# Kernel optimization log

Measured on AMD Instinct MI355X. Metric: run time of the kernel, lower is better.

The kernel has to match this reference:

```python
import jax, jax.numpy as jnp
import numpy as np


def gcn_conv(x, row, col, W, b, n_nodes):
    """PyG GCNConv: x' = D^-1/2 (A+I) D^-1/2 (x W) + b, with self-loops in row/col."""
    xw = x @ W  # [N, out]
    deg = jax.ops.segment_sum(jnp.ones_like(col, dtype=xw.dtype), col, num_segments=n_nodes)
    d_inv_sqrt = jnp.where(deg > 0, jax.lax.rsqrt(deg), 0.0)
    norm = d_inv_sqrt[row] * d_inv_sqrt[col]  # [E+N]
    msgs = norm[:, None] * xw[row]            # gather + scale
    out = jax.ops.segment_sum(msgs, col, num_segments=n_nodes)  # scatter-add to dst
    return out + b


def setup_inputs() -> dict:
    key = jax.random.key(0)
    ks = jax.random.split(key, 8)
    N, E = 100000, 1600000
    d_in, d_h, d_out = 128, 128, 64
    x = jax.random.normal(ks[0], (N, d_in), dtype=jnp.float32)
    edge_index = jax.random.randint(ks[1], (2, E), 0, N, dtype=jnp.int32)
    s = 1.0 / np.sqrt(d_in)
    W1 = jax.random.uniform(ks[2], (d_in, d_h), jnp.float32, -s, s)
    b1 = jnp.zeros((d_h,), jnp.float32)
    sh = 1.0 / np.sqrt(d_h)
    W2 = jax.random.uniform(ks[3], (d_h, d_h), jnp.float32, -sh, sh)
    b2 = jnp.zeros((d_h,), jnp.float32)
    W3 = jax.random.uniform(ks[4], (d_h, d_out), jnp.float32, -sh, sh)
    b3 = jnp.zeros((d_out,), jnp.float32)
    return {"x": x, "edge_index": edge_index, "W1": W1, "b1": b1,
            "W2": W2, "b2": b2, "W3": W3, "b3": b3}


def reference(x, edge_index, W1, b1, W2, b2, W3, b3):
    n_nodes = x.shape[0]
    loops = jnp.arange(n_nodes, dtype=edge_index.dtype)
    row = jnp.concatenate([edge_index[0], loops])  # src (with self-loops)
    col = jnp.concatenate([edge_index[1], loops])  # dst (with self-loops)
    # dropout p=0.0 / eval mode -> identity, omitted
    h = jax.nn.relu(gcn_conv(x, row, col, W1, b1, n_nodes))
    h = jax.nn.relu(gcn_conv(h, row, col, W2, b2, n_nodes))
    out = gcn_conv(h, row, col, W3, b3, n_nodes)
    return out
```

## Files before the change

### kernel.cpp

```cpp
#include <hip/hip_runtime.h>
#include <hip/hip_fp16.h>

typedef _Float16 half8 __attribute__((ext_vector_type(8)));
typedef float floatx4 __attribute__((ext_vector_type(4)));

#define NCH 128
#define TILE 2048
#define CSLOT 48
#define MAXNB 1024
#define MAXCH 1024
#define OVFCAP 65536

__global__ __launch_bounds__(256) void wconv_k(const float* __restrict__ W1,
                                               const float* __restrict__ W2,
                                               const float* __restrict__ W3,
                                               __half* __restrict__ Wt1,
                                               __half* __restrict__ Wt2,
                                               __half* __restrict__ Wt3,
                                               int* __restrict__ ovfcnt) {
    int idx = blockIdx.x * 256 + threadIdx.x;
    if (idx < 16384) {
        int k = idx >> 7, nn = idx & 127;
        Wt1[nn * 128 + k] = __float2half(W1[idx]);
    } else if (idx < 32768) {
        int j = idx - 16384;
        int k = j >> 7, nn = j & 127;
        Wt2[nn * 128 + k] = __float2half(W2[j]);
    } else if (idx < 40960) {
        int j = idx - 32768;
        int k = j >> 6, nn = j & 63;
        Wt3[nn * 128 + k] = __float2half(W3[j]);
    } else if (idx == 40960) {
        *ovfcnt = 0;
    }
}

__global__ __launch_bounds__(256) void part_k(const int* __restrict__ row,
                                              const int* __restrict__ col, int E,
                                              int chunk, int NB,
                                              int* __restrict__ stg_d,
                                              int* __restrict__ stg_s,
                                              int* __restrict__ cnts,
                                              unsigned long long* __restrict__ ovf,
                                              int* __restrict__ ovfcnt) {
    __shared__ int bd[NCH][CSLOT];
    __shared__ int bs[NCH][CSLOT];
    __shared__ int lcnt[NCH];
    __shared__ int lpref[NCH + 1];
    int tid = threadIdx.x;
    int b = blockIdx.x;
    for (int i = tid; i < NCH; i += 256) lcnt[i] = 0;
    __syncthreads();

    int i0 = b * TILE + tid * 8;
    int sv[8], dv[8];
    int nv = 0;
    if (i0 + 7 < E && (E & 3) == 0) {
        int4 r0 = *(const int4*)(row + i0);
        int4 r1 = *(const int4*)(row + i0 + 4);
        int4 c0 = *(const int4*)(col + i0);
        int4 c1 = *(const int4*)(col + i0 + 4);
        sv[0] = r0.x; sv[1] = r0.y; sv[2] = r0.z; sv[3] = r0.w;
        sv[4] = r1.x; sv[5] = r1.y; sv[6] = r1.z; sv[7] = r1.w;
        dv[0] = c0.x; dv[1] = c0.y; dv[2] = c0.z; dv[3] = c0.w;
        dv[4] = c1.x; dv[5] = c1.y; dv[6] = c1.z; dv[7] = c1.w;
        nv = 8;
    } else {
#pragma unroll
        for (int j = 0; j < 8; j++) {
            if (i0 + j < E) { sv[nv] = row[i0 + j]; dv[nv] = col[i0 + j]; nv++; }
        }
    }
#pragma unroll 8
    for (int j = 0; j < nv; j++) {
        int d = dv[j], s = sv[j];
        int c = d / chunk;
        int r = atomicAdd(&lcnt[c], 1);
        if (r < CSLOT) {
            bd[c][r] = d;
            bs[c][r] = s;
        } else {
            int o = atomicAdd(ovfcnt, 1);
            if (o < OVFCAP)
                ovf[o] = ((unsigned long long)(unsigned)d << 32) | (unsigned)s;
        }
    }
    __syncthreads();
    if (tid == 0) {
        int a = 0;
#pragma unroll
        for (int c = 0; c < NCH; c++) {
            lpref[c] = a;
            a += min(lcnt[c], CSLOT);
        }
        lpref[NCH] = a;
    }
    __syncthreads();
    for (int c = tid; c < NCH; c += 256) cnts[(size_t)c * NB + b] = min(lcnt[c], CSLOT);
    int total = lpref[NCH];
    for (int f = tid; f < total; f += 256) {
        int lo = 0, hi = NCH;
        while (hi - lo > 1) {
            int mid = (lo + hi) >> 1;
            if (lpref[mid] <= f) lo = mid; else hi = mid;
        }
        int slot = f - lpref[lo];
        size_t cell = ((size_t)lo * NB + b) * CSLOT;
        stg_d[cell + slot] = bd[lo][slot];
        stg_s[cell + slot] = bs[lo][slot];
    }
}

__global__ __launch_bounds__(256) void degcnt_k(const int* __restrict__ stg_d,
                                                const int* __restrict__ cnts, int NB,
                                                int N, int chunk,
                                                const unsigned long long* __restrict__ ovf,
                                                const int* __restrict__ ovfcnt,
                                                int* __restrict__ deg,
                                                float* __restrict__ dinv) {
    __shared__ int hist[MAXCH];
    __shared__ int lc[MAXNB];
    int c = blockIdx.x, tid = threadIdx.x;
    int dlo = c * chunk;
    int dhi = min(N, dlo + chunk);
    int csz = dhi - dlo;
    if (csz <= 0) return;
    for (int i = tid; i < csz; i += 256) hist[i] = 1;
    for (int i = tid; i < NB; i += 256) lc[i] = cnts[(size_t)c * NB + i];
    __syncthreads();
    for (int b0 = tid >> 4; b0 < NB; b0 += 16) {
        int cnt = lc[b0];
        size_t base = ((size_t)c * NB + b0) * CSLOT;
        for (int slot = tid & 15; slot < cnt; slot += 16) {
            int d = stg_d[base + slot];
            atomicAdd(&hist[d - dlo], 1);
        }
    }
    __syncthreads();
    int oc = min(*ovfcnt, OVFCAP);
    for (int i = tid; i < oc; i += 256) {
        int d = (int)(ovf[i] >> 32);
        if (d >= dlo && d < dhi) atomicAdd(&hist[d - dlo], 1);
    }
    __syncthreads();
    for (int i = tid; i < csz; i += 256) {
        int dg = hist[i];
        deg[dlo + i] = dg;
        dinv[dlo + i] = rsqrtf((float)dg);
    }
}

__global__ __launch_bounds__(256) void scan_p1(const int* __restrict__ deg, int n,
                                               int* __restrict__ bsum) {
    __shared__ int lds[256];
    int t = threadIdx.x;
    int base = blockIdx.x * 1024 + t * 4;
    int s = 0;
#pragma unroll
    for (int i = 0; i < 4; i++) {
        int idx = base + i;
        if (idx < n) s += deg[idx];
    }
    lds[t] = s;
    __syncthreads();
    for (int o = 128; o > 0; o >>= 1) {
        if (t < o) lds[t] += lds[t + o];
        __syncthreads();
    }
    if (t == 0) bsum[blockIdx.x] = lds[0];
}

__global__ __launch_bounds__(256) void scan_p2(int* __restrict__ bsum, int nb) {
    __shared__ int lds[256];
    int t = threadIdx.x;
    int v = (t < nb) ? bsum[t] : 0;
    lds[t] = v;
    __syncthreads();
    for (int o = 1; o < 256; o <<= 1) {
        int tmp = 0;
        if (t >= o) tmp = lds[t - o];
        __syncthreads();
        lds[t] += tmp;
        __syncthreads();
    }
    if (t < nb) bsum[t] = lds[t] - v;
}

__global__ __launch_bounds__(256) void scan_p3(const int* __restrict__ deg, int n,
                                               const int* __restrict__ bsum,
                                               int* __restrict__ cptr) {
    __shared__ int lds[256];
    int t = threadIdx.x;
    int base = blockIdx.x * 1024 + t * 4;
    int v[4];
    int s = 0;
#pragma unroll
    for (int i = 0; i < 4; i++) {
        int idx = base + i;
        v[i] = (idx < n) ? deg[idx] : 0;
        s += v[i];
    }
    lds[t] = s;
    __syncthreads();
    for (int o = 1; o < 256; o <<= 1) {
        int tmp = 0;
        if (t >= o) tmp = lds[t - o];
        __syncthreads();
        lds[t] += tmp;
        __syncthreads();
    }
    int off = bsum[blockIdx.x] + (lds[t] - s);
#pragma unroll
    for (int i = 0; i < 4; i++) {
        int idx = base + i;
        if (idx < n) {
            cptr[idx] = off;
            off += v[i];
            if (idx == n - 1) cptr[n] = off;
        }
    }
}

__global__ __launch_bounds__(256) void fill3_k(const int* __restrict__ stg_d,
                                               const int* __restrict__ stg_s,
                                               const int* __restrict__ cnts, int NB,
                                               const int* __restrict__ cptr,
                                               int N, int chunk,
                                               const unsigned long long* __restrict__ ovf,
                                               const int* __restrict__ ovfcnt,
                                               int* __restrict__ meta) {
    __shared__ int cur[MAXCH];
    __shared__ int lc[MAXNB];
    int c = blockIdx.x, tid = threadIdx.x;
    int dlo = c * chunk;
    int dhi = min(N, dlo + chunk);
    int csz = dhi - dlo;
    if (csz <= 0) return;
    for (int i = tid; i < csz; i += 256) cur[i] = cptr[dlo + i];
    for (int i = tid; i < NB; i += 256) lc[i] = cnts[(size_t)c * NB + i];
    __syncthreads();
    for (int b0 = tid >> 4; b0 < NB; b0 += 16) {
        int cnt = lc[b0];
        size_t base = ((size_t)c * NB + b0) * CSLOT;
        for (int slot = tid & 15; slot < cnt; slot += 16) {
            int d = stg_d[base + slot];
            int s = stg_s[base + slot];
            int p = atomicAdd(&cur[d - dlo], 1);
            meta[p] = s;
        }
    }
    for (int i = tid; i < csz; i += 256) {
        int p = atomicAdd(&cur[i], 1);
        meta[p] = dlo + i;
    }
    int oc = min(*ovfcnt, OVFCAP);
    for (int i = tid; i < oc; i += 256) {
        unsigned long long v = ovf[i];
        int d = (int)(v >> 32);
        if (d >= dlo && d < dhi) {
            int p = atomicAdd(&cur[d - dlo], 1);
            meta[p] = (int)(v & 0xffffffffull);
        }
    }
}

template <typename AT, int DOUT>
__global__ __launch_bounds__(256) void gemm_mfma(const AT* __restrict__ A,
                                                 const __half* __restrict__ Wt,
                                                 const float* __restrict__ dinv,
                                                 __half* __restrict__ C, int n) {
    constexpr int CT = DOUT / 16;
    constexpr int WP = 136;
    __shared__ _Float16 ldsW[DOUT * WP];
    int tid = threadIdx.x;
    int lane = tid & 63;
    int wid = tid >> 6;
    for (int i = tid; i < DOUT * 16; i += 256) {
        int nrow = i >> 4;
        int kc = (i & 15) * 8;
        *(half8*)(&ldsW[nrow * WP + kc]) =
            *(const half8*)((const _Float16*)Wt + nrow * 128 + kc);
    }
    __syncthreads();
    int rwb = blockIdx.x * 128 + wid * 32;
    int m = lane & 15;
    int quad = lane >> 4;
    floatx4 acc[2][CT];
#pragma unroll
    for (int t = 0; t < 2; t++)
#pragma unroll
        for (int c = 0; c < CT; c++) acc[t][c] = (floatx4){0.f, 0.f, 0.f, 0.f};

#pragma unroll
    for (int kq = 0; kq < 4; kq++) {
        int k0 = kq * 32 + quad * 8;
        half8 afr[2];
#pragma unroll
        for (int t = 0; t < 2; t++) {
            int r = rwb + t * 16 + m;
            r = r < n ? r : n - 1;
            const AT* ap = A + (size_t)r * 128 + k0;
            if constexpr (sizeof(AT) == 2) {
                afr[t] = *(const half8*)ap;
            } else {
                float4 f0 = *(const float4*)ap;
                float4 f1 = *(const float4*)(ap + 4);
                half8 h;
                h[0] = (_Float16)f0.x; h[1] = (_Float16)f0.y;
                h[2] = (_Float16)f0.z; h[3] = (_Float16)f0.w;
                h[4] = (_Float16)f1.x; h[5] = (_Float16)f1.y;
                h[6] = (_Float16)f1.z; h[7] = (_Float16)f1.w;
                afr[t] = h;
            }
        }
#pragma unroll
        for (int c = 0; c < CT; c++) {
            half8 bfr = *(const half8*)(&ldsW[(c * 16 + m) * WP + k0]);
#pragma unroll
            for (int t = 0; t < 2; t++)
                acc[t][c] =
                    __builtin_amdgcn_mfma_f32_16x16x32_f16(afr[t], bfr, acc[t][c], 0, 0, 0);
        }
    }
#pragma unroll
    for (int t = 0; t < 2; t++) {
#pragma unroll
        for (int reg = 0; reg < 4; reg++) {
            int r = rwb + t * 16 + quad * 4 + reg;
            if (r < n) {
                float dv = dinv[r];
#pragma unroll
                for (int c = 0; c < CT; c++)
                    C[(size_t)r * DOUT + c * 16 + m] = __float2half(acc[t][c][reg] * dv);
            }
        }
    }
}

template <int D, bool RELU, typename OT>
__global__ __launch_bounds__(256) void aggregate_k(const __half* __restrict__ xw,
                                                   const int* __restrict__ ptr,
                                                   const int* __restrict__ meta,
                                                   const float* __restrict__ bias,
                                                   const float* __restrict__ dinv,
                                                   OT* __restrict__ out, int n) {
    constexpr int GS = D / 8;
    constexpr int EPW = 64 / GS;
    constexpr int UNR = (EPW == 4) ? 4 : 2;
    __shared__ int smeta[4][64];
    int lane = threadIdx.x & 63;
    int wid = threadIdx.x >> 6;
    int node = blockIdx.x * 4 + wid;
    if (node >= n) return;
    int e0 = ptr[node], e1 = ptr[node + 1];
    float dv = dinv[node];
    int sub = lane / GS;
    int cg = lane % GS;
    const _Float16* xp = (const _Float16*)xw + cg * 8;
    float acc[8];
#pragma unroll
    for (int i = 0; i < 8; i++) acc[i] = 0.f;

    for (int base = e0; base < e1; base += 64) {
        int cnt = min(e1 - base, 64);
        if (lane < cnt) smeta[wid][lane] = meta[base + lane];
        for (int j = 0; j < cnt; j += UNR * EPW) {
            int sreg[UNR];
            float mk[UNR];
#pragma unroll
            for (int u = 0; u < UNR; u++) {
                int e = j + u * EPW + sub;
                bool val = e < cnt;
                sreg[u] = smeta[wid][val ? e : 0];
                mk[u] = val ? 1.f : 0.f;
            }
            half8 vreg[UNR];
#pragma unroll
            for (int u = 0; u < UNR; u++)
                vreg[u] = *(const half8*)(xp + (size_t)sreg[u] * D);
#pragma unroll
            for (int u = 0; u < UNR; u++)
#pragma unroll
                for (int i = 0; i < 8; i++)
                    acc[i] = fmaf(mk[u], (float)vreg[u][i], acc[i]);
        }
    }
#pragma unroll
    for (int off = GS; off < 64; off <<= 1) {
#pragma unroll
        for (int i = 0; i < 8; i++) acc[i] += __shfl_xor(acc[i], off, 64);
    }
    if (lane < GS) {
        float4 bb0 = *(const float4*)(bias + cg * 8);
        float4 bb1 = *(const float4*)(bias + cg * 8 + 4);
        float r[8];
        r[0] = acc[0] * dv + bb0.x; r[1] = acc[1] * dv + bb0.y;
        r[2] = acc[2] * dv + bb0.z; r[3] = acc[3] * dv + bb0.w;
        r[4] = acc[4] * dv + bb1.x; r[5] = acc[5] * dv + bb1.y;
        r[6] = acc[6] * dv + bb1.z; r[7] = acc[7] * dv + bb1.w;
        if (RELU) {
#pragma unroll
            for (int i = 0; i < 8; i++) r[i] = fmaxf(r[i], 0.f);
        }
        if constexpr (sizeof(OT) == 2) {
            half8 h;
#pragma unroll
            for (int i = 0; i < 8; i++) h[i] = (_Float16)r[i];
            *(half8*)((_Float16*)out + (size_t)node * D + cg * 8) = h;
        } else {
            float* op = (float*)out + (size_t)node * D + cg * 8;
            *(float4*)op = make_float4(r[0], r[1], r[2], r[3]);
            *(float4*)(op + 4) = make_float4(r[4], r[5], r[6], r[7]);
        }
    }
}

extern "C" void kernel_launch(void* const* d_in, const int* in_sizes, int n_in,
                              void* d_out, int out_size, void* d_ws, size_t ws_size,
                              hipStream_t stream) {
    const float* x = (const float*)d_in[0];
    const int* ei = (const int*)d_in[1];
    const float* W1 = (const float*)d_in[2];
    const float* b1 = (const float*)d_in[3];
    const float* W2 = (const float*)d_in[4];
    const float* b2 = (const float*)d_in[5];
    const float* W3 = (const float*)d_in[6];
    const float* b3 = (const float*)d_in[7];
    float* out = (float*)d_out;
    int N = in_sizes[0] / 128;
    int E = in_sizes[1] / 2;
    const int* row = ei;
    const int* col = ei + E;
    int T = E + N;

    char* w = (char*)d_ws;
    size_t off = 0;
    auto alloc = [&](size_t bytes) -> void* {
        void* p = w + off;
        off = (off + bytes + 511) & ~(size_t)511;
        return p;
    };
    __half* bufH = (__half*)alloc((size_t)N * 128 * 2);
    __half* bufA = (__half*)alloc((size_t)N * 128 * 2);
    __half* Wt1 = (__half*)alloc(16384 * 2);
    __half* Wt2 = (__half*)alloc(16384 * 2);
    __half* Wt3 = (__half*)alloc(8192 * 2);
    int* deg = (int*)alloc((size_t)N * 4);
    float* dinv = (float*)alloc((size_t)N * 4);
    int* cptr = (int*)alloc((size_t)(N + 1) * 4);
    int* meta = (int*)alloc((size_t)T * 4);
    int* bsum = (int*)alloc(4096);
    int* ovfcnt = (int*)alloc(64);
    unsigned long long* ovf = (unsigned long long*)alloc((size_t)OVFCAP * 8);
    int NB = (E + TILE - 1) / TILE;
    int* cnts = (int*)alloc((size_t)NCH * NB * 4);
    int chunk = (N + NCH - 1) / NCH;

    int* stg_d = (int*)bufH;
    int* stg_s = stg_d + (size_t)NCH * NB * CSLOT;

    int nb = (N + 1023) / 1024;
    wconv_k<<<161, 256, 0, stream>>>(W1, W2, W3, Wt1, Wt2, Wt3, ovfcnt);
    part_k<<<NB, 256, 0, stream>>>(row, col, E, chunk, NB, stg_d, stg_s, cnts, ovf, ovfcnt);
    degcnt_k<<<NCH, 256, 0, stream>>>(stg_d, cnts, NB, N, chunk, ovf, ovfcnt, deg, dinv);
    scan_p1<<<nb, 256, 0, stream>>>(deg, N, bsum);
    scan_p2<<<1, 256, 0, stream>>>(bsum, nb);
    scan_p3<<<nb, 256, 0, stream>>>(deg, N, bsum, cptr);
    fill3_k<<<NCH, 256, 0, stream>>>(stg_d, stg_s, cnts, NB, cptr, N, chunk, ovf, ovfcnt, meta);

    int gb = (N + 127) / 128;
    int ab = (N + 3) / 4;
    gemm_mfma<float, 128><<<gb, 256, 0, stream>>>(x, Wt1, dinv, bufH, N);
    aggregate_k<128, true, __half><<<ab, 256, 0, stream>>>(bufH, cptr, meta, b1, dinv, bufA, N);
    gemm_mfma<__half, 128><<<gb, 256, 0, stream>>>(bufA, Wt2, dinv, bufH, N);
    aggregate_k<128, true, __half><<<ab, 256, 0, stream>>>(bufH, cptr, meta, b2, dinv, bufA, N);
    gemm_mfma<__half, 64><<<gb, 256, 0, stream>>>(bufA, Wt3, dinv, bufH, N);
    aggregate_k<64, false, float><<<ab, 256, 0, stream>>>(bufH, cptr, meta, b3, dinv, out, N);
}
```

Measured before the change: 395.6 us.

## Fuse degree scan into CSR histogram/fill kernels and drop aggregation masks

Replaces the three-kernel prefix scan with per-chunk degree sums computed in the histogram kernel and a local scan inside the fill kernel, cutting three launches. Both CSR kernels now use 512 threads per block. The aggregation loop no longer multiplies by a validity mask. Out-of-range edge slots instead point at a zero row appended after the GEMM output, which the GEMM writes. Staging buffers are split across bufH and bufA, and the extra padding row adds a little memory.

After: 376.1 us. 1.05x faster.

```diff
diff --git a/kernel.cpp b/kernel.cpp
--- a/kernel.cpp
+++ b/kernel.cpp
@@ -111,150 +111,123 @@
     }
 }
 
-__global__ __launch_bounds__(256) void degcnt_k(const int* __restrict__ stg_d,
-                                                const int* __restrict__ cnts, int NB,
-                                                int N, int chunk,
-                                                const unsigned long long* __restrict__ ovf,
-                                                const int* __restrict__ ovfcnt,
-                                                int* __restrict__ deg,
-                                                float* __restrict__ dinv) {
+__global__ __launch_bounds__(512) void csr_hist_k(const int* __restrict__ stg_d,
+                                                  const int* __restrict__ cnts, int NB,
+                                                  int N, int chunk,
+                                                  const unsigned long long* __restrict__ ovf,
+                                                  const int* __restrict__ ovfcnt,
+                                                  int* __restrict__ deg,
+                                                  float* __restrict__ dinv,
+                                                  int* __restrict__ csum) {
     __shared__ int hist[MAXCH];
-    __shared__ int lc[MAXNB];
+    __shared__ int red[512];
+    int c = blockIdx.x, tid = threadIdx.x;
+    int dlo = c * chunk;
+    int dhi = min(N, dlo + chunk);
+    int csz = dhi - dlo;
+    if (csz <= 0) {
+        if (tid == 0) csum[c] = 0;
+        return;
+    }
+    for (int i = tid; i < csz; i += 512) hist[i] = 1;
+    __syncthreads();
+    for (int b0 = tid >> 4; b0 < NB; b0 += 32) {
+        int cnt = cnts[(size_t)c * NB + b0];
+        size_t base = ((size_t)c * NB + b0) * CSLOT;
+        for (int slot = tid & 15; slot < cnt; slot += 16)
+            atomicAdd(&hist[stg_d[base + slot] - dlo], 1);
+    }
+    int oc = min(*ovfcnt, OVFCAP);
+    for (int i = tid; i < oc; i += 512) {
+        int d = (int)(ovf[i] >> 32);
+        if (d >= dlo && d < dhi) atomicAdd(&hist[d - dlo], 1);
+    }
+    __syncthreads();
+    int t = 0;
+    for (int i = tid; i < csz; i += 512) {
+        int dg = hist[i];
+        deg[dlo + i] = dg;
+        dinv[dlo + i] = rsqrtf((float)dg);
+        t += dg;
+    }
+    red[tid] = t;
+    __syncthreads();
+    for (int o = 256; o > 0; o >>= 1) {
+        if (tid < o) red[tid] += red[tid + o];
+        __syncthreads();
+    }
+    if (tid == 0) csum[c] = red[0];
+}
+
+__global__ __launch_bounds__(512) void csr_fill_k(const int* __restrict__ stg_d,
+                                                  const int* __restrict__ stg_s,
+                                                  const int* __restrict__ cnts, int NB,
+                                                  const int* __restrict__ deg,
+                                                  const int* __restrict__ csum,
+                                                  int N, int chunk,
+                                                  const unsigned long long* __restrict__ ovf,
+                                                  const int* __restrict__ ovfcnt,
+                                                  int* __restrict__ cptr,
+                                                  int* __restrict__ meta) {
+    __shared__ int cur[MAXCH];
+    __shared__ int sc[512];
     int c = blockIdx.x, tid = threadIdx.x;
     int dlo = c * chunk;
     int dhi = min(N, dlo + chunk);
     int csz = dhi - dlo;
     if (csz <= 0) return;
-    for (int i = tid; i < csz; i += 256) hist[i] = 1;
-    for (int i = tid; i < NB; i += 256) lc[i] = cnts[(size_t)c * NB + i];
-    __syncthreads();
-    for (int b0 = tid >> 4; b0 < NB; b0 += 16) {
-        int cnt = lc[b0];
+
+    sc[tid] = (tid < NCH && tid < c) ? csum[tid] : 0;
+    __syncthreads();
+    for (int o = 256; o > 0; o >>= 1) {
+        if (tid < o) sc[tid] += sc[tid + o];
+        __syncthreads();
+    }
+    int cbase = sc[0];
+    __syncthreads();
+
+    int i0 = tid * 2;
+    int v0 = (i0 < csz) ? deg[dlo + i0] : 0;
+    int v1 = (i0 + 1 < csz) ? deg[dlo + i0 + 1] : 0;
+    int s = v0 + v1;
+    sc[tid] = s;
+    __syncthreads();
+    for (int o = 1; o < 512; o <<= 1) {
+        int tmp = 0;
+        if (tid >= o) tmp = sc[tid - o];
+        __syncthreads();
+        sc[tid] += tmp;
+        __syncthreads();
+    }
+    int off = cbase + sc[tid] - s;
+    if (i0 < csz) {
+        cur[i0] = off;
+        cptr[dlo + i0] = off;
+        off += v0;
+        if (i0 + 1 < csz) {
+            cur[i0 + 1] = off;
+            cptr[dlo + i0 + 1] = off;
+        }
+    }
+    if (dhi == N && tid == 511) cptr[N] = cbase + sc[511];
+    __syncthreads();
+
+    for (int b0 = tid >> 4; b0 < NB; b0 += 32) {
+        int cnt = cnts[(size_t)c * NB + b0];
         size_t base = ((size_t)c * NB + b0) * CSLOT;
         for (int slot = tid & 15; slot < cnt; slot += 16) {
             int d = stg_d[base + slot];
-            atomicAdd(&hist[d - dlo], 1);
-        }
-    }
-    __syncthreads();
-    int oc = min(*ovfcnt, OVFCAP);
-    for (int i = tid; i < oc; i += 256) {
-        int d = (int)(ovf[i] >> 32);
-        if (d >= dlo && d < dhi) atomicAdd(&hist[d - dlo], 1);
-    }
-    __syncthreads();
-    for (int i = tid; i < csz; i += 256) {
-        int dg = hist[i];
-        deg[dlo + i] = dg;
-        dinv[dlo + i] = rsqrtf((float)dg);
-    }
-}
-
-__global__ __launch_bounds__(256) void scan_p1(const int* __restrict__ deg, int n,
-                                               int* __restrict__ bsum) {
-    __shared__ int lds[256];
-    int t = threadIdx.x;
-    int base = blockIdx.x * 1024 + t * 4;
-    int s = 0;
-#pragma unroll
-    for (int i = 0; i < 4; i++) {
-        int idx = base + i;
-        if (idx < n) s += deg[idx];
-    }
-    lds[t] = s;
-    __syncthreads();
-    for (int o = 128; o > 0; o >>= 1) {
-        if (t < o) lds[t] += lds[t + o];
-        __syncthreads();
-    }
-    if (t == 0) bsum[blockIdx.x] = lds[0];
-}
-
-__global__ __launch_bounds__(256) void scan_p2(int* __restrict__ bsum, int nb) {
-    __shared__ int lds[256];
-    int t = threadIdx.x;
-    int v = (t < nb) ? bsum[t] : 0;
-    lds[t] = v;
-    __syncthreads();
-    for (int o = 1; o < 256; o <<= 1) {
-        int tmp = 0;
-        if (t >= o) tmp = lds[t - o];
-        __syncthreads();
-        lds[t] += tmp;
-        __syncthreads();
-    }
-    if (t < nb) bsum[t] = lds[t] - v;
-}
-
-__global__ __launch_bounds__(256) void scan_p3(const int* __restrict__ deg, int n,
-                                               const int* __restrict__ bsum,
-                                               int* __restrict__ cptr) {
-    __shared__ int lds[256];
-    int t = threadIdx.x;
-    int base = blockIdx.x * 1024 + t * 4;
-    int v[4];
-    int s = 0;
-#pragma unroll
-    for (int i = 0; i < 4; i++) {
-        int idx = base + i;
-        v[i] = (idx < n) ? deg[idx] : 0;
-        s += v[i];
-    }
-    lds[t] = s;
-    __syncthreads();
-    for (int o = 1; o < 256; o <<= 1) {
-        int tmp = 0;
-        if (t >= o) tmp = lds[t - o];
-        __syncthreads();
-        lds[t] += tmp;
-        __syncthreads();
-    }
-    int off = bsum[blockIdx.x] + (lds[t] - s);
-#pragma unroll
-    for (int i = 0; i < 4; i++) {
-        int idx = base + i;
-        if (idx < n) {
-            cptr[idx] = off;
-            off += v[i];
-            if (idx == n - 1) cptr[n] = off;
-        }
-    }
-}
-
-__global__ __launch_bounds__(256) void fill3_k(const int* __restrict__ stg_d,
-                                               const int* __restrict__ stg_s,
-                                               const int* __restrict__ cnts, int NB,
-                                               const int* __restrict__ cptr,
-                                               int N, int chunk,
-                                               const unsigned long long* __restrict__ ovf,
-                                               const int* __restrict__ ovfcnt,
-                                               int* __restrict__ meta) {
-    __shared__ int cur[MAXCH];
-    __shared__ int lc[MAXNB];
-    int c = blockIdx.x, tid = threadIdx.x;
-    int dlo = c * chunk;
-    int dhi = min(N, dlo + chunk);
-    int csz = dhi - dlo;
-    if (csz <= 0) return;
-    for (int i = tid; i < csz; i += 256) cur[i] = cptr[dlo + i];
-    for (int i = tid; i < NB; i += 256) lc[i] = cnts[(size_t)c * NB + i];
-    __syncthreads();
-    for (int b0 = tid >> 4; b0 < NB; b0 += 16) {
-        int cnt = lc[b0];
-        size_t base = ((size_t)c * NB + b0) * CSLOT;
-        for (int slot = tid & 15; slot < cnt; slot += 16) {
-            int d = stg_d[base + slot];
-            int s = stg_s[base + slot];
+            int sv = stg_s[base + slot];
             int p = atomicAdd(&cur[d - dlo], 1);
-            meta[p] = s;
-        }
-    }
-    for (int i = tid; i < csz; i += 256) {
+            meta[p] = sv;
+        }
+    }
+    for (int i = tid; i < csz; i += 512) {
         int p = atomicAdd(&cur[i], 1);
         meta[p] = dlo + i;
     }
     int oc = min(*ovfcnt, OVFCAP);
-    for (int i = tid; i < oc; i += 256) {
+    for (int i = tid; i < oc; i += 512) {
         unsigned long long v = ovf[i];
         int d = (int)(v >> 32);
         if (d >= dlo && d < dhi) {
@@ -334,6 +307,10 @@
                     C[(size_t)r * DOUT + c * 16 + m] = __float2half(acc[t][c][reg] * dv);
             }
         }
+    }
+    if (blockIdx.x == 0 && tid < DOUT / 8) {
+        half8 z = (half8){0, 0, 0, 0, 0, 0, 0, 0};
+        *(half8*)((_Float16*)C + (size_t)n * DOUT + tid * 8) = z;
     }
 }
 
@@ -366,13 +343,11 @@
         if (lane < cnt) smeta[wid][lane] = meta[base + lane];
         for (int j = 0; j < cnt; j += UNR * EPW) {
             int sreg[UNR];
-            float mk[UNR];
 #pragma unroll
             for (int u = 0; u < UNR; u++) {
                 int e = j + u * EPW + sub;
-                bool val = e < cnt;
-                sreg[u] = smeta[wid][val ? e : 0];
-                mk[u] = val ? 1.f : 0.f;
+                int t = smeta[wid][e];
+                sreg[u] = (e < cnt) ? t : n;
             }
             half8 vreg[UNR];
 #pragma unroll
@@ -382,7 +357,7 @@
             for (int u = 0; u < UNR; u++)
 #pragma unroll
                 for (int i = 0; i < 8; i++)
-                    acc[i] = fmaf(mk[u], (float)vreg[u][i], acc[i]);
+                    acc[i] += (float)vreg[u][i];
         }
     }
 #pragma unroll
@@ -440,7 +415,7 @@
         off = (off + bytes + 511) & ~(size_t)511;
         return p;
     };
-    __half* bufH = (__half*)alloc((size_t)N * 128 * 2);
+    __half* bufH = (__half*)alloc((size_t)(N + 1) * 128 * 2);
     __half* bufA = (__half*)alloc((size_t)N * 128 * 2);
     __half* Wt1 = (__half*)alloc(16384 * 2);
     __half* Wt2 = (__half*)alloc(16384 * 2);
@@ -449,7 +424,7 @@
     float* dinv = (float*)alloc((size_t)N * 4);
     int* cptr = (int*)alloc((size_t)(N + 1) * 4);
     int* meta = (int*)alloc((size_t)T * 4);
-    int* bsum = (int*)alloc(4096);
+    int* csum = (int*)alloc(NCH * 4);
     int* ovfcnt = (int*)alloc(64);
     unsigned long long* ovf = (unsigned long long*)alloc((size_t)OVFCAP * 8);
     int NB = (E + TILE - 1) / TILE;
@@ -457,16 +432,13 @@
     int chunk = (N + NCH - 1) / NCH;
 
     int* stg_d = (int*)bufH;
-    int* stg_s = stg_d + (size_t)NCH * NB * CSLOT;
-
-    int nb = (N + 1023) / 1024;
+    int* stg_s = (int*)bufA;
+
     wconv_k<<<161, 256, 0, stream>>>(W1, W2, W3, Wt1, Wt2, Wt3, ovfcnt);
     part_k<<<NB, 256, 0, stream>>>(row, col, E, chunk, NB, stg_d, stg_s, cnts, ovf, ovfcnt);
-    degcnt_k<<<NCH, 256, 0, stream>>>(stg_d, cnts, NB, N, chunk, ovf, ovfcnt, deg, dinv);
-    scan_p1<<<nb, 256, 0, stream>>>(deg, N, bsum);
-    scan_p2<<<1, 256, 0, stream>>>(bsum, nb);
-    scan_p3<<<nb, 256, 0, stream>>>(deg, N, bsum, cptr);
-    fill3_k<<<NCH, 256, 0, stream>>>(stg_d, stg_s, cnts, NB, cptr, N, chunk, ovf, ovfcnt, meta);
+    csr_hist_k<<<NCH, 512, 0, stream>>>(stg_d, cnts, NB, N, chunk, ovf, ovfcnt, deg, dinv, csum);
+    csr_fill_k<<<NCH, 512, 0, stream>>>(stg_d, stg_s, cnts, NB, deg, csum, N, chunk, ovf,
+                                        ovfcnt, cptr, meta);
 
     int gb = (N + 127) / 128;
     int ab = (N + 3) / 4;
```
